# Kernel optimization log

Hardware: AMD Instinct MI355X
Metric: run time of the kernel (lower is better)

## Reference

```python
import jax, jax.numpy as jnp
import numpy as np
import math

B, S, OBS, ACT = 64, 256, 96, 29
D, H, L, FF = 512, 8, 8, 2048
HD = D // H
EPS = 1e-5

def _ln(x, g, b):
    m = jnp.mean(x, axis=-1, keepdims=True)
    v = jnp.mean((x - m) ** 2, axis=-1, keepdims=True)
    return (x - m) * jax.lax.rsqrt(v + EPS) * g + b

def _pos_encoding():
    pos = jnp.arange(S, dtype=jnp.float32)[:, None]
    div = jnp.exp(jnp.arange(0, D, 2, dtype=jnp.float32) * (-math.log(10000.0) / D))
    pe = jnp.zeros((S, D), dtype=jnp.float32)
    pe = pe.at[:, 0::2].set(jnp.sin(pos * div))
    pe = pe.at[:, 1::2].set(jnp.cos(pos * div))
    return pe

def setup_inputs() -> dict:
    key = jax.random.key(0)
    ks = iter(jax.random.split(key, 64))
    def w(shape, scale=0.02):
        return jax.random.normal(next(ks), shape, dtype=jnp.float32) * scale
    inp = {
        "observations": jax.random.normal(next(ks), (B, S, OBS), dtype=jnp.float32),
        "W_in": w((OBS, D)), "b_in": jnp.zeros((D,)),
        "g_in": jnp.ones((D,)), "be_in": jnp.zeros((D,)),
        "Wq": w((L, D, D)), "bq": jnp.zeros((L, D)),
        "Wk": w((L, D, D)), "bk": jnp.zeros((L, D)),
        "Wv": w((L, D, D)), "bv": jnp.zeros((L, D)),
        "Wo": w((L, D, D)), "bo": jnp.zeros((L, D)),
        "g1": jnp.ones((L, D)), "be1": jnp.zeros((L, D)),
        "W1": w((L, D, FF)), "b1": jnp.zeros((L, FF)),
        "W2": w((L, FF, D)), "b2": jnp.zeros((L, D)),
        "g2": jnp.ones((L, D)), "be2": jnp.zeros((L, D)),
        "Wp1": w((D, D // 2)), "bp1": jnp.zeros((D // 2,)),
        "gp1": jnp.ones((D // 2,)), "bep1": jnp.zeros((D // 2,)),
        "Wp2": w((D // 2, D // 4)), "bp2": jnp.zeros((D // 4,)),
        "gp2": jnp.ones((D // 4,)), "bep2": jnp.zeros((D // 4,)),
        "Wp3": w((D // 4, ACT)), "bp3": jnp.zeros((ACT,)),
        "action_scale": jnp.ones((ACT,)), "action_bias": jnp.zeros((ACT,)),
    }
    return inp

def _forward(observations, W_in, b_in, g_in, be_in, Wq, bq, Wk, bk, Wv, bv, Wo, bo,
             g1, be1, W1, b1, W2, b2, g2, be2,
             Wp1, bp1, gp1, bep1, Wp2, bp2, gp2, bep2, Wp3, bp3,
             action_scale, action_bias):
    gelu = lambda x: jax.nn.gelu(x, approximate=False)
    # input projection + LN + GELU (dropout = identity in eval)
    x = gelu(_ln(observations @ W_in + b_in, g_in, be_in))
    x = x + _pos_encoding()[None, :, :]  # [B,S,D]
    scale = 1.0 / math.sqrt(HD)
    for l in range(L):
        q = (x @ Wq[l] + bq[l]).reshape(B, S, H, HD)
        k = (x @ Wk[l] + bk[l]).reshape(B, S, H, HD)
        v = (x @ Wv[l] + bv[l]).reshape(B, S, H, HD)
        scores = jnp.einsum('bqhd,bkhd->bhqk', q, k) * scale
        attn = jax.nn.softmax(scores, axis=-1)
        o = jnp.einsum('bhqk,bkhd->bqhd', attn, v).reshape(B, S, D)
        x = _ln(x + (o @ Wo[l] + bo[l]), g1[l], be1[l])
        h = gelu(x @ W1[l] + b1[l])
        x = _ln(x + (h @ W2[l] + b2[l]), g2[l], be2[l])
    y = gelu(_ln(x @ Wp1 + bp1, gp1, bep1))
    y = gelu(_ln(y @ Wp2 + bp2, gp2, bep2))
    actions = jnp.tanh(y @ Wp3 + bp3)
    return actions * action_scale + action_bias

def reference(observations, W_in, b_in, g_in, be_in, Wq, bq, Wk, bk, Wv, bv, Wo, bo,
              g1, be1, W1, b1, W2, b2, g2, be2,
              Wp1, bp1, gp1, bep1, Wp2, bp2, gp2, bep2, Wp3, bp3,
              action_scale, action_bias):
    return _forward(observations, W_in, b_in, g_in, be_in, Wq, bq, Wk, bk, Wv, bv, Wo, bo,
                    g1, be1, W1, b1, W2, b2, g2, be2,
                    Wp1, bp1, gp1, bep1, Wp2, bp2, gp2, bep2, Wp3, bp3,
                    action_scale, action_bias)
```

## Files before the change

### kernel.cpp

```cpp
#include <hip/hip_runtime.h>

typedef unsigned short u16;
typedef unsigned int u32;
typedef __attribute__((ext_vector_type(8))) __bf16 bf16x8;
typedef __attribute__((ext_vector_type(4))) float f32x4;

#define B_ 64
#define S_ 256
#define OBS_ 96
#define ACT_ 29
#define D_ 512
#define H_ 8
#define L_ 8
#define FF_ 2048
#define HD_ 64
#define NTOK (B_ * S_)
#define QKV3 (3 * D_)

__device__ __forceinline__ u16 f2bf(float f) {
    u32 u = __float_as_uint(f);
    u += 0x7FFFu + ((u >> 16) & 1u);
    return (u16)(u >> 16);
}
__device__ __forceinline__ float bf2f(u16 h) {
    return __uint_as_float(((u32)h) << 16);
}
__device__ __forceinline__ u16 f2h(float f) {
    _Float16 h = (_Float16)f;
    u16 u; __builtin_memcpy(&u, &h, 2); return u;
}
__device__ __forceinline__ float h2f(u16 u) {
    _Float16 h; __builtin_memcpy(&h, &u, 2); return (float)h;
}
__device__ __forceinline__ float gelu_f(float x) {
    const float k1 = 2.3022121f;
    const float k2 = 0.10294451f;
    float x2 = x * x;
    float arg = x * __builtin_fmaf(x2, k2, k1);
    float e = exp2f(arg);
    float r = __builtin_amdgcn_rcpf(1.0f + e);
    return __builtin_fmaf(-x, r, x);
}
__device__ __forceinline__ void gld_lds16(const u16* g, u16* l) {
    __builtin_amdgcn_global_load_lds(
        (const __attribute__((address_space(1))) unsigned int*)g,
        (__attribute__((address_space(3))) unsigned int*)l, 16, 0, 0);
}

__global__ __launch_bounds__(256) void transpose_bf16_kernel(
    const float* __restrict__ src, u16* __restrict__ dst, int K, int N,
    size_t srcStride, size_t dstStride)
{
    __shared__ float tile[32][33];
    int n0 = blockIdx.x * 32, k0 = blockIdx.y * 32;
    const float* s = src + (size_t)blockIdx.z * srcStride;
    u16* d = dst + (size_t)blockIdx.z * dstStride;
    int tx = threadIdx.x, ty = threadIdx.y;
    for (int i = 0; i < 32; i += 8)
        tile[ty + i][tx] = s[(size_t)(k0 + ty + i) * N + n0 + tx];
    __syncthreads();
    for (int i = 0; i < 32; i += 8)
        d[(size_t)(n0 + ty + i) * K + k0 + tx] = f2bf(tile[tx][ty + i]);
}

__global__ __launch_bounds__(256) void concat_bias_kernel(
    const float* __restrict__ bq, const float* __restrict__ bk,
    const float* __restrict__ bv, float* __restrict__ dst)
{
    int i = blockIdx.x * 256 + threadIdx.x;
    int l = i / QKV3, r = i - l * QKV3;
    float v;
    if (r < D_)            v = bq[l * D_ + r];
    else if (r < 2 * D_)   v = bk[l * D_ + r - D_];
    else                   v = bv[l * D_ + r - 2 * D_];
    dst[i] = v;
}

__global__ __launch_bounds__(256) void in_gemm_kernel(
    const float* __restrict__ obs, const float* __restrict__ Win,
    const float* __restrict__ b_in, float* __restrict__ outp)
{
    __shared__ float As[OBS_][68];
    __shared__ float Bs[OBS_][68];
    int m0 = blockIdx.y * 64, n0 = blockIdx.x * 64;
    int t = threadIdx.x;
    #pragma unroll
    for (int i = 0; i < 24; i++) {
        int idx = i * 256 + t;
        int m = idx / OBS_, kk = idx - m * OBS_;
        As[kk][m] = obs[(size_t)(m0 + m) * OBS_ + kk];
    }
    #pragma unroll
    for (int i = 0; i < 24; i++) {
        int idx = i * 256 + t;
        int kk = idx >> 6, n = idx & 63;
        Bs[kk][n] = Win[(size_t)kk * D_ + n0 + n];
    }
    __syncthreads();
    int tm = t >> 4, tn = t & 15;
    float acc[4][4] = {};
    for (int kk = 0; kk < OBS_; kk++) {
        float4 a = *(const float4*)&As[kk][tm * 4];
        float4 b = *(const float4*)&Bs[kk][tn * 4];
        const float av[4] = {a.x, a.y, a.z, a.w};
        const float bv[4] = {b.x, b.y, b.z, b.w};
        #pragma unroll
        for (int r = 0; r < 4; r++)
            #pragma unroll
            for (int c = 0; c < 4; c++) acc[r][c] += av[r] * bv[c];
    }
    #pragma unroll
    for (int r = 0; r < 4; r++)
        #pragma unroll
        for (int c = 0; c < 4; c++) {
            int col = n0 + tn * 4 + c;
            outp[(size_t)(m0 + tm * 4 + r) * D_ + col] = acc[r][c] + b_in[col];
        }
}

template <int EPI, int TN, bool SPLITK>
__global__ __launch_bounds__(256, 3) void gemm_bt_kernel(
    const u16* __restrict__ A, const u16* __restrict__ BT,
    const float* __restrict__ bias, void* __restrict__ C,
    void* __restrict__ C2, int M, int N, int K, int kLen)
{
    constexpr int NI = TN / 32;
    constexpr int NB = TN / 32;
    __shared__ __align__(16) u16 smem[128 * 64 + TN * 64];
    u16* As = smem;
    u16* Bs = smem + 128 * 64;
    int bx = blockIdx.x;
    int m0 = (bx & 127) * 128, n0 = (bx >> 7) * TN;
    int z = SPLITK ? blockIdx.z : 0;
    int kStart = z * kLen;
    int t = threadIdx.x;
    int lane = t & 63, w = t >> 6;
    int wm = w >> 1, wn = w & 1;
    int l15 = lane & 15, quad = lane >> 4;

    int offC[4]; u16* lA[4];
    #pragma unroll
    for (int i = 0; i < 4; i++) {
        int ci = t + i * 256;
        int r = ci >> 3, s = ci & 7, gc = s ^ (r & 7);
        offC[i] = r * K + gc * 8;
        lA[i] = &As[ci * 8];
    }
    const u16* Abase = A + (size_t)m0 * K + kStart;
    const u16* Bbase = BT + (size_t)n0 * K + kStart;

    int aoff[2][4], boff[2][NI];
    #pragma unroll
    for (int kh = 0; kh < 2; kh++) {
        #pragma unroll
        for (int mi = 0; mi < 4; mi++) {
            int row = wm * 64 + mi * 16 + l15;
            aoff[kh][mi] = row * 64 + (((kh * 4 + quad) ^ (row & 7)) * 8);
        }
        #pragma unroll
        for (int ni = 0; ni < NI; ni++) {
            int row = wn * (TN / 2) + ni * 16 + l15;
            boff[kh][ni] = row * 64 + (((kh * 4 + quad) ^ (row & 7)) * 8);
        }
    }

    f32x4 acc[4][NI];
    f32x4 zero = {0.f, 0.f, 0.f, 0.f};
    #pragma unroll
    for (int mi = 0; mi < 4; mi++)
        #pragma unroll
        for (int ni = 0; ni < NI; ni++) acc[mi][ni] = zero;

    for (int kk = 0; kk < kLen; kk += 64) {
        __syncthreads();
        #pragma unroll
        for (int i = 0; i < 4; i++) gld_lds16(Abase + offC[i], lA[i]);
        #pragma unroll
        for (int i = 0; i < NB; i++) gld_lds16(Bbase + offC[i], lA[i] + 128 * 64);
        Abase += 64; Bbase += 64;
        __syncthreads();
        #pragma unroll
        for (int kh = 0; kh < 2; kh++) {
            bf16x8 a[4], b[NI];
            #pragma unroll
            for (int mi = 0; mi < 4; mi++)
                a[mi] = *(const bf16x8*)&As[aoff[kh][mi]];
            #pragma unroll
            for (int ni = 0; ni < NI; ni++)
                b[ni] = *(const bf16x8*)&Bs[boff[kh][ni]];
            #pragma unroll
            for (int mi = 0; mi < 4; mi++)
                #pragma unroll
                for (int ni = 0; ni < NI; ni++)
                    acc[mi][ni] = __builtin_amdgcn_mfma_f32_16x16x32_bf16(
                        a[mi], b[ni], acc[mi][ni], 0, 0, 0);
        }
    }

    bool partial = SPLITK && (z == 1);
    if (EPI == 2) {
        #pragma unroll
        for (int ni = 0; ni < NI; ni++) {
            int col = n0 + wn * (TN / 2) + ni * 16 + l15;
            float bv = partial ? 0.f : bias[col];
            #pragma unroll
            for (int mi = 0; mi < 4; mi++) {
                int rbase = m0 + wm * 64 + mi * 16 + quad * 4;
                f32x4 v = acc[mi][ni];
                #pragma unroll
                for (int r = 0; r < 4; r++)
                    ((float*)C)[(size_t)(rbase + r) * N + col] = v[r] + bv;
            }
        }
    } else {
        __syncthreads();
        u16* Ct = smem;
        #pragma unroll
        for (int ni = 0; ni < NI; ni++) {
            int colt = wn * (TN / 2) + ni * 16 + l15;
            float bv = partial ? 0.f : bias[n0 + colt];
            #pragma unroll
            for (int mi = 0; mi < 4; mi++) {
                int rbase = wm * 64 + mi * 16 + quad * 4;
                f32x4 v = acc[mi][ni];
                #pragma unroll
                for (int r = 0; r < 4; r++) {
                    float y = v[r] + bv;
                    if (EPI == 1) y = gelu_f(y);
                    u16 hv = (EPI == 3) ? f2h(y) : f2bf(y);
                    int row = rbase + r;
                    int cc = colt >> 3;
                    Ct[row * TN + (((cc ^ (row & 7)) * 8) | (colt & 7))] = hv;
                }
            }
        }
        __syncthreads();
        u16* dst = partial ? (u16*)C2 : (u16*)C;
        constexpr int CPR = TN / 8;
        #pragma unroll
        for (int i = 0; i < TN / 16; i++) {
            int ch = t + i * 256;
            int row = ch / CPR, cc = ch % CPR;
            uint4 vv = *(const uint4*)&Ct[row * TN + ((cc ^ (row & 7)) * 8)];
            *(uint4*)(dst + (size_t)(m0 + row) * N + n0 + cc * 8) = vv;
        }
    }
}

__global__ __launch_bounds__(256) void attn_kernel(
    const u16* __restrict__ qkv, u16* __restrict__ o)
{
    __shared__ __align__(16) u16 kvs[S_ * HD_];
    __shared__ __align__(16) u16 P[4 * 16 * S_];
    int bx = blockIdx.x;
    int qc = bx & 3;
    int h = (bx >> 2) & 7;
    int b = bx >> 5;
    int t = threadIdx.x;
    int lane = t & 63, w = t >> 6;
    int l15 = lane & 15, quad = lane >> 4;
    size_t rowb = (size_t)b * S_;

    {
        const u16* src = qkv + (rowb + t) * QKV3 + D_ + h * HD_;
        int sw = t & 7;
        #pragma unroll
        for (int j = 0; j < 8; j++)
            *(uint4*)&kvs[t * HD_ + ((j ^ sw) * 8)] = *(const uint4*)(src + j * 8);
    }
    bf16x8 aQ[2];
    {
        int qrow = qc * 64 + w * 16 + l15;
        const u16* src = qkv + (rowb + qrow) * QKV3 + h * HD_ + quad * 8;
        aQ[0] = *(const bf16x8*)(src);
        aQ[1] = *(const bf16x8*)(src + 32);
    }
    __syncthreads();

    f32x4 sc[16];
    #pragma unroll
    for (int nc = 0; nc < 16; nc++) {
        f32x4 acc = {0.f, 0.f, 0.f, 0.f};
        int row = nc * 16 + l15;
        int s0 = quad ^ (row & 7);
        bf16x8 b0 = *(const bf16x8*)&kvs[row * HD_ + s0 * 8];
        bf16x8 b1 = *(const bf16x8*)&kvs[row * HD_ + (s0 ^ 4) * 8];
        acc = __builtin_amdgcn_mfma_f32_16x16x32_bf16(aQ[0], b0, acc, 0, 0, 0);
        acc = __builtin_amdgcn_mfma_f32_16x16x32_bf16(aQ[1], b1, acc, 0, 0, 0);
        sc[nc] = acc;
    }
    const float scale = 0.125f;
    float rmax[4], rinv[4];
    #pragma unroll
    for (int r = 0; r < 4; r++) {
        float mx = -1e30f;
        #pragma unroll
        for (int nc = 0; nc < 16; nc++) mx = fmaxf(mx, sc[nc][r]);
        for (int off = 1; off < 16; off <<= 1) mx = fmaxf(mx, __shfl_xor(mx, off));
        rmax[r] = mx * scale;
    }
    #pragma unroll
    for (int r = 0; r < 4; r++) {
        float sum = 0.f;
        #pragma unroll
        for (int nc = 0; nc < 16; nc++) {
            float p = __expf(sc[nc][r] * scale - rmax[r]);
            sc[nc][r] = p;
            sum += p;
        }
        for (int off = 1; off < 16; off <<= 1) sum += __shfl_xor(sum, off);
        rinv[r] = 1.0f / sum;
    }
    #pragma unroll
    for (int nc = 0; nc < 16; nc++)
        #pragma unroll
        for (int r = 0; r < 4; r++) {
            int prow = quad * 4 + r;
            int col = nc * 16 + l15;
            int slot = (col >> 3) ^ (prow & 7);
            P[w * 4096 + prow * 256 + slot * 8 + (col & 7)] =
                f2bf(sc[nc][r] * rinv[r]);
        }
    __syncthreads();

    {
        const u16* src = qkv + (rowb + t) * QKV3 + 2 * D_ + h * HD_;
        int chunkc = t >> 3, bytec = t & 7;
        #pragma unroll
        for (int dj = 0; dj < 8; dj++) {
            uint4 x = *(const uint4*)(src + dj * 8);
            const u16* xs = (const u16*)&x;
            #pragma unroll
            for (int i = 0; i < 8; i++) {
                int vrow = dj * 8 + i;
                kvs[vrow * 256 + ((chunkc ^ (vrow & 7)) * 8) + bytec] = xs[i];
            }
        }
    }
    __syncthreads();

    f32x4 accO[4];
    f32x4 zero = {0.f, 0.f, 0.f, 0.f};
    #pragma unroll
    for (int nt = 0; nt < 4; nt++) accO[nt] = zero;
    for (int ks = 0; ks < 8; ks++) {
        int ch = ks * 4 + quad;
        bf16x8 aP = *(const bf16x8*)&P[w * 4096 + l15 * 256 + ((ch ^ (l15 & 7)) * 8)];
        #pragma unroll
        for (int nt = 0; nt < 4; nt++) {
            int vrow = nt * 16 + l15;
            bf16x8 bV = *(const bf16x8*)&kvs[vrow * 256 + ((ch ^ (vrow & 7)) * 8)];
            accO[nt] = __builtin_amdgcn_mfma_f32_16x16x32_bf16(aP, bV, accO[nt], 0, 0, 0);
        }
    }
    __syncthreads();
    u16* Ot = P;
    #pragma unroll
    for (int nt = 0; nt < 4; nt++)
        #pragma unroll
        for (int r = 0; r < 4; r++) {
            int row = w * 16 + quad * 4 + r;
            int col = nt * 16 + l15;
            int cc = col >> 3;
            Ot[row * 64 + (((cc ^ (row & 7)) * 8) | (col & 7))] = f2bf(accO[nt][r]);
        }
    __syncthreads();
    #pragma unroll
    for (int i = 0; i < 2; i++) {
        int ch = t + i * 256;
        int row = ch >> 3, cc = ch & 7;
        uint4 vv = *(const uint4*)&Ot[row * 64 + ((cc ^ (row & 7)) * 8)];
        *(uint4*)(o + (rowb + qc * 64 + row) * D_ + h * HD_ + cc * 8) = vv;
    }
}

template <int WIDTH, int INK, bool RES, bool GELU, bool PE, bool SUM2>
__global__ __launch_bounds__(WIDTH) void ln_kernel(
    const void* __restrict__ in, const void* __restrict__ in2,
    const u16* __restrict__ res,
    const float* __restrict__ g, const float* __restrict__ b,
    u16* __restrict__ out)
{
    __shared__ float rs[8], rq[8];
    int row = blockIdx.x;
    int t = threadIdx.x;
    size_t base = (size_t)row * WIDTH;
    float v = (INK == 0) ? ((const float*)in)[base + t]
                         : h2f(((const u16*)in)[base + t]);
    if (SUM2) v += (INK == 0) ? ((const float*)in2)[base + t]
                              : h2f(((const u16*)in2)[base + t]);
    if (RES) v += bf2f(res[base + t]);
    float sm = v, sq = v * v;
    for (int off = 32; off; off >>= 1) {
        sm += __shfl_xor(sm, off);
        sq += __shfl_xor(sq, off);
    }
    constexpr int NW = WIDTH / 64;
    if ((t & 63) == 0) { rs[t >> 6] = sm; rq[t >> 6] = sq; }
    __syncthreads();
    float ts = 0.f, tq = 0.f;
    #pragma unroll
    for (int i = 0; i < NW; i++) { ts += rs[i]; tq += rq[i]; }
    float mean = ts / (float)WIDTH;
    float var = tq / (float)WIDTH - mean * mean;
    float rstd = rsqrtf(var + 1e-5f);
    float y = (v - mean) * rstd * g[t] + b[t];
    if (GELU) y = gelu_f(y);
    if (PE) {
        const float c = -9.210340371976184f / (float)D_;
        int s = row & (S_ - 1);
        int i2 = t >> 1;
        float ang = (float)s * __expf((float)(2 * i2) * c);
        y += (t & 1) ? __cosf(ang) : __sinf(ang);
    }
    out[base + t] = f2bf(y);
}

__global__ __launch_bounds__(256) void head_kernel(
    const u16* __restrict__ y2, const float* __restrict__ W,
    const float* __restrict__ bias, const float* __restrict__ scl,
    const float* __restrict__ bs, float* __restrict__ out)
{
    __shared__ float Ws[128 * ACT_];
    __shared__ u16 Ys[8 * 128];
    int t = threadIdx.x;
    for (int i = t; i < 128 * ACT_; i += 256) Ws[i] = W[i];
    int r0 = blockIdx.x * 8;
    for (int i = t; i < 8 * 128; i += 256) Ys[i] = y2[(size_t)r0 * 128 + i];
    __syncthreads();
    int lr = t >> 5, c = t & 31;
    if (c < ACT_) {
        float acc = bias[c];
        for (int kk = 0; kk < 128; kk++)
            acc += bf2f(Ys[lr * 128 + kk]) * Ws[kk * ACT_ + c];
        float y = tanhf(acc);
        out[(size_t)(r0 + lr) * ACT_ + c] = y * scl[c] + bs[c];
    }
}

extern "C" void kernel_launch(void* const* d_in, const int* in_sizes, int n_in,
                              void* d_out, int out_size, void* d_ws, size_t ws_size,
                              hipStream_t stream)
{
    const float* obs   = (const float*)d_in[0];
    const float* W_in  = (const float*)d_in[1];
    const float* b_in  = (const float*)d_in[2];
    const float* g_in  = (const float*)d_in[3];
    const float* be_in = (const float*)d_in[4];
    const float* Wq  = (const float*)d_in[5];
    const float* bq  = (const float*)d_in[6];
    const float* Wk  = (const float*)d_in[7];
    const float* bk  = (const float*)d_in[8];
    const float* Wv  = (const float*)d_in[9];
    const float* bv  = (const float*)d_in[10];
    const float* Wo  = (const float*)d_in[11];
    const float* bo  = (const float*)d_in[12];
    const float* g1  = (const float*)d_in[13];
    const float* be1 = (const float*)d_in[14];
    const float* W1  = (const float*)d_in[15];
    const float* b1  = (const float*)d_in[16];
    const float* W2  = (const float*)d_in[17];
    const float* b2  = (const float*)d_in[18];
    const float* g2  = (const float*)d_in[19];
    const float* be2 = (const float*)d_in[20];
    const float* Wp1  = (const float*)d_in[21];
    const float* bp1  = (const float*)d_in[22];
    const float* gp1  = (const float*)d_in[23];
    const float* bep1 = (const float*)d_in[24];
    const float* Wp2  = (const float*)d_in[25];
    const float* bp2  = (const float*)d_in[26];
    const float* gp2  = (const float*)d_in[27];
    const float* bep2 = (const float*)d_in[28];
    const float* Wp3  = (const float*)d_in[29];
    const float* bp3  = (const float*)d_in[30];
    const float* ascl = (const float*)d_in[31];
    const float* abias = (const float*)d_in[32];

    char* ws = (char*)d_ws;
    size_t off = 0;
    auto alloc = [&](size_t bytes) {
        void* p = ws + off;
        off += (bytes + 255) & ~(size_t)255;
        return p;
    };
    u16* WQKVT = (u16*)alloc((size_t)L_ * QKV3 * D_ * 2);
    u16* WOT   = (u16*)alloc((size_t)L_ * D_ * D_ * 2);
    u16* W1T   = (u16*)alloc((size_t)L_ * D_ * FF_ * 2);
    u16* W2T   = (u16*)alloc((size_t)L_ * FF_ * D_ * 2);
    u16* WP1T  = (u16*)alloc((size_t)D_ * (D_ / 2) * 2);
    u16* WP2T  = (u16*)alloc((size_t)(D_ / 2) * (D_ / 4) * 2);
    float* bqkv = (float*)alloc((size_t)L_ * QKV3 * 4);
    u16* x_bf = (u16*)alloc((size_t)NTOK * D_ * 2);
    float* tmp = (float*)alloc((size_t)NTOK * D_ * 4);
    char* regionA = (char*)alloc((size_t)NTOK * FF_ * 2);
    size_t base_need = off;
    char* tmp2 = ws + base_need;
    bool split = (ws_size >= base_need + (size_t)NTOK * D_ * 2);
    (void)in_sizes; (void)n_in; (void)out_size;

    u16* qkvbuf = (u16*)(regionA);
    u16* obuf = (u16*)(regionA + (size_t)NTOK * QKV3 * 2);
    u16* hbuf = (u16*)(regionA);
    u16* y1_bf = (u16*)(regionA);
    u16* y2_bf = (u16*)(regionA + (32u << 20));

    dim3 tb(32, 8);
    size_t DD = (size_t)D_ * D_;
    transpose_bf16_kernel<<<dim3(16, 16, L_), tb, 0, stream>>>(
        Wq, WQKVT, D_, D_, DD, (size_t)QKV3 * D_);
    transpose_bf16_kernel<<<dim3(16, 16, L_), tb, 0, stream>>>(
        Wk, WQKVT + DD, D_, D_, DD, (size_t)QKV3 * D_);
    transpose_bf16_kernel<<<dim3(16, 16, L_), tb, 0, stream>>>(
        Wv, WQKVT + 2 * DD, D_, D_, DD, (size_t)QKV3 * D_);
    transpose_bf16_kernel<<<dim3(16, 16, L_), tb, 0, stream>>>(
        Wo, WOT, D_, D_, DD, DD);
    transpose_bf16_kernel<<<dim3(64, 16, L_), tb, 0, stream>>>(
        W1, W1T, D_, FF_, (size_t)D_ * FF_, (size_t)D_ * FF_);
    transpose_bf16_kernel<<<dim3(16, 64, L_), tb, 0, stream>>>(
        W2, W2T, FF_, D_, (size_t)D_ * FF_, (size_t)D_ * FF_);
    transpose_bf16_kernel<<<dim3(8, 16, 1), tb, 0, stream>>>(
        Wp1, WP1T, D_, D_ / 2, 0, 0);
    transpose_bf16_kernel<<<dim3(4, 8, 1), tb, 0, stream>>>(
        Wp2, WP2T, D_ / 2, D_ / 4, 0, 0);
    concat_bias_kernel<<<L_ * QKV3 / 256, 256, 0, stream>>>(bq, bk, bv, bqkv);

    in_gemm_kernel<<<dim3(D_ / 64, NTOK / 64), 256, 0, stream>>>(
        obs, W_in, b_in, tmp);
    ln_kernel<D_, 0, false, true, true, false><<<NTOK, D_, 0, stream>>>(
        tmp, nullptr, nullptr, g_in, be_in, x_bf);

    const int MG = NTOK / 128;
    for (int l = 0; l < L_; l++) {
        const u16* wqkvt = WQKVT + (size_t)l * QKV3 * D_;
        const u16* wot = WOT + (size_t)l * DD;
        const u16* w1t = W1T + (size_t)l * D_ * FF_;
        const u16* w2t = W2T + (size_t)l * FF_ * D_;

        gemm_bt_kernel<0, 128, false><<<MG * (QKV3 / 128), 256, 0, stream>>>(
            x_bf, wqkvt, bqkv + l * QKV3, qkvbuf, nullptr, NTOK, QKV3, D_, D_);
        attn_kernel<<<B_ * H_ * (S_ / 64), 256, 0, stream>>>(qkvbuf, obuf);
        if (split) {
            gemm_bt_kernel<3, 128, true><<<dim3(MG * 4, 1, 2), 256, 0, stream>>>(
                obuf, wot, bo + l * D_, tmp, tmp2, NTOK, D_, D_, D_ / 2);
            ln_kernel<D_, 1, true, false, false, true><<<NTOK, D_, 0, stream>>>(
                tmp, tmp2, x_bf, g1 + l * D_, be1 + l * D_, x_bf);
        } else {
            gemm_bt_kernel<2, 128, false><<<MG * 4, 256, 0, stream>>>(
                obuf, wot, bo + l * D_, tmp, nullptr, NTOK, D_, D_, D_);
            ln_kernel<D_, 0, true, false, false, false><<<NTOK, D_, 0, stream>>>(
                tmp, nullptr, x_bf, g1 + l * D_, be1 + l * D_, x_bf);
        }
        gemm_bt_kernel<1, 128, false><<<MG * (FF_ / 128), 256, 0, stream>>>(
            x_bf, w1t, b1 + l * FF_, hbuf, nullptr, NTOK, FF_, D_, D_);
        if (split) {
            gemm_bt_kernel<3, 128, true><<<dim3(MG * 4, 1, 2), 256, 0, stream>>>(
                hbuf, w2t, b2 + l * D_, tmp, tmp2, NTOK, D_, FF_, FF_ / 2);
            ln_kernel<D_, 1, true, false, false, true><<<NTOK, D_, 0, stream>>>(
                tmp, tmp2, x_bf, g2 + l * D_, be2 + l * D_, x_bf);
        } else {
            gemm_bt_kernel<2, 128, false><<<MG * 4, 256, 0, stream>>>(
                hbuf, w2t, b2 + l * D_, tmp, nullptr, NTOK, D_, FF_, FF_);
            ln_kernel<D_, 0, true, false, false, false><<<NTOK, D_, 0, stream>>>(
                tmp, nullptr, x_bf, g2 + l * D_, be2 + l * D_, x_bf);
        }
    }

    if (split) {
        gemm_bt_kernel<3, 64, true><<<dim3(MG * 4, 1, 2), 256, 0, stream>>>(
            x_bf, WP1T, bp1, tmp, tmp2, NTOK, D_ / 2, D_, D_ / 2);
        ln_kernel<D_ / 2, 1, false, true, false, true><<<NTOK, D_ / 2, 0, stream>>>(
            tmp, tmp2, nullptr, gp1, bep1, y1_bf);
        gemm_bt_kernel<3, 64, true><<<dim3(MG * 2, 1, 2), 256, 0, stream>>>(
            y1_bf, WP2T, bp2, tmp, tmp2, NTOK, D_ / 4, D_ / 2, D_ / 4);
        ln_kernel<D_ / 4, 1, false, true, false, true><<<NTOK, D_ / 4, 0, stream>>>(
            tmp, tmp2, nullptr, gp2, bep2, y2_bf);
    } else {
        gemm_bt_kernel<2, 64, false><<<MG * 4, 256, 0, stream>>>(
            x_bf, WP1T, bp1, tmp, nullptr, NTOK, D_ / 2, D_, D_);
        ln_kernel<D_ / 2, 0, false, true, false, false><<<NTOK, D_ / 2, 0, stream>>>(
            tmp, nullptr, nullptr, gp1, bep1, y1_bf);
        gemm_bt_kernel<2, 64, false><<<MG * 2, 256, 0, stream>>>(
            y1_bf, WP2T, bp2, tmp, nullptr, NTOK, D_ / 4, D_ / 2, D_ / 2);
        ln_kernel<D_ / 4, 0, false, true, false, false><<<NTOK, D_ / 4, 0, stream>>>(
            tmp, nullptr, nullptr, gp2, bep2, y2_bf);
    }
    head_kernel<<<NTOK / 8, 256, 0, stream>>>(
        y2_bf, Wp3, bp3, ascl, abias, (float*)d_out);
}
```

Baseline: 2.196 ms.

## Vectorize layernorm, defer softmax normalization, use native bf16 convert and paired GELU

LayerNorm now processes four elements per thread with vector loads and stores and packs several rows into each 256-thread block. This cuts block count and the shared-memory reduction for narrow rows. Attention applies the softmax reciprocal to the 64-wide output instead of to every probability. f2bf uses the hardware bf16 conversion, and the GEMM epilogue computes GELU on float pairs to encourage packed math. These are several unrelated micro-optimizations on non-GEMM costs, with small rounding differences (P is stored unnormalized in bf16).

```diff
diff --git a/kernel.cpp b/kernel.cpp
--- a/kernel.cpp
+++ b/kernel.cpp
@@ -4,6 +4,7 @@
 typedef unsigned int u32;
 typedef __attribute__((ext_vector_type(8))) __bf16 bf16x8;
 typedef __attribute__((ext_vector_type(4))) float f32x4;
+typedef __attribute__((ext_vector_type(2))) float f32x2;
 
 #define B_ 64
 #define S_ 256
@@ -18,9 +19,8 @@
 #define QKV3 (3 * D_)
 
 __device__ __forceinline__ u16 f2bf(float f) {
-    u32 u = __float_as_uint(f);
-    u += 0x7FFFu + ((u >> 16) & 1u);
-    return (u16)(u >> 16);
+    __bf16 h = (__bf16)f;
+    u16 u; __builtin_memcpy(&u, &h, 2); return u;
 }
 __device__ __forceinline__ float bf2f(u16 h) {
     return __uint_as_float(((u32)h) << 16);
@@ -40,6 +40,20 @@
     float e = exp2f(arg);
     float r = __builtin_amdgcn_rcpf(1.0f + e);
     return __builtin_fmaf(-x, r, x);
+}
+__device__ __forceinline__ f32x2 gelu2(f32x2 x) {
+    const float k1 = 2.3022121f;
+    const float k2 = 0.10294451f;
+    f32x2 x2 = x * x;
+    f32x2 arg = x * (x2 * k2 + k1);
+    f32x2 e;
+    e.x = exp2f(arg.x);
+    e.y = exp2f(arg.y);
+    f32x2 one_e = e + 1.0f;
+    f32x2 r;
+    r.x = __builtin_amdgcn_rcpf(one_e.x);
+    r.y = __builtin_amdgcn_rcpf(one_e.y);
+    return x - x * r;
 }
 __device__ __forceinline__ void gld_lds16(const u16* g, u16* l) {
     __builtin_amdgcn_global_load_lds(
@@ -223,11 +237,15 @@
             for (int mi = 0; mi < 4; mi++) {
                 int rbase = wm * 64 + mi * 16 + quad * 4;
                 f32x4 v = acc[mi][ni];
+                f32x2 y01 = {v[0], v[1]};
+                f32x2 y23 = {v[2], v[3]};
+                y01 = y01 + bv;
+                y23 = y23 + bv;
+                if (EPI == 1) { y01 = gelu2(y01); y23 = gelu2(y23); }
+                const float ys[4] = {y01.x, y01.y, y23.x, y23.y};
                 #pragma unroll
                 for (int r = 0; r < 4; r++) {
-                    float y = v[r] + bv;
-                    if (EPI == 1) y = gelu_f(y);
-                    u16 hv = (EPI == 3) ? f2h(y) : f2bf(y);
+                    u16 hv = (EPI == 3) ? f2h(ys[r]) : f2bf(ys[r]);
                     int row = rbase + r;
                     int cc = colt >> 3;
                     Ct[row * TN + (((cc ^ (row & 7)) * 8) | (colt & 7))] = hv;
@@ -318,8 +336,7 @@
             int prow = quad * 4 + r;
             int col = nc * 16 + l15;
             int slot = (col >> 3) ^ (prow & 7);
-            P[w * 4096 + prow * 256 + slot * 8 + (col & 7)] =
-                f2bf(sc[nc][r] * rinv[r]);
+            P[w * 4096 + prow * 256 + slot * 8 + (col & 7)] = f2bf(sc[nc][r]);
         }
     __syncthreads();
 
@@ -362,7 +379,8 @@
             int row = w * 16 + quad * 4 + r;
             int col = nt * 16 + l15;
             int cc = col >> 3;
-            Ot[row * 64 + (((cc ^ (row & 7)) * 8) | (col & 7))] = f2bf(accO[nt][r]);
+            Ot[row * 64 + (((cc ^ (row & 7)) * 8) | (col & 7))] =
+                f2bf(accO[nt][r] * rinv[r]);
         }
     __syncthreads();
     #pragma unroll
@@ -375,45 +393,93 @@
 }
 
 template <int WIDTH, int INK, bool RES, bool GELU, bool PE, bool SUM2>
-__global__ __launch_bounds__(WIDTH) void ln_kernel(
+__global__ __launch_bounds__(256) void ln_kernel(
     const void* __restrict__ in, const void* __restrict__ in2,
     const u16* __restrict__ res,
     const float* __restrict__ g, const float* __restrict__ b,
     u16* __restrict__ out)
 {
-    __shared__ float rs[8], rq[8];
-    int row = blockIdx.x;
+    constexpr int T = WIDTH / 4;
+    constexpr int R = 256 / T;
+    __shared__ float rs[R][2], rq[R][2];
     int t = threadIdx.x;
-    size_t base = (size_t)row * WIDTH;
-    float v = (INK == 0) ? ((const float*)in)[base + t]
-                         : h2f(((const u16*)in)[base + t]);
-    if (SUM2) v += (INK == 0) ? ((const float*)in2)[base + t]
-                              : h2f(((const u16*)in2)[base + t]);
-    if (RES) v += bf2f(res[base + t]);
-    float sm = v, sq = v * v;
-    for (int off = 32; off; off >>= 1) {
-        sm += __shfl_xor(sm, off);
-        sq += __shfl_xor(sq, off);
-    }
-    constexpr int NW = WIDTH / 64;
-    if ((t & 63) == 0) { rs[t >> 6] = sm; rq[t >> 6] = sq; }
-    __syncthreads();
-    float ts = 0.f, tq = 0.f;
-    #pragma unroll
-    for (int i = 0; i < NW; i++) { ts += rs[i]; tq += rq[i]; }
-    float mean = ts / (float)WIDTH;
-    float var = tq / (float)WIDTH - mean * mean;
+    int r = t / T, j = t % T;
+    int row = blockIdx.x * R + r;
+    size_t base = (size_t)row * WIDTH + j * 4;
+    float v[4];
+    if (INK == 0) {
+        float4 x = *(const float4*)((const float*)in + base);
+        v[0] = x.x; v[1] = x.y; v[2] = x.z; v[3] = x.w;
+    } else {
+        uint2 x = *(const uint2*)((const u16*)in + base);
+        const u16* xs = (const u16*)&x;
+        #pragma unroll
+        for (int i = 0; i < 4; i++) v[i] = h2f(xs[i]);
+    }
+    if (SUM2) {
+        if (INK == 0) {
+            float4 x = *(const float4*)((const float*)in2 + base);
+            v[0] += x.x; v[1] += x.y; v[2] += x.z; v[3] += x.w;
+        } else {
+            uint2 x = *(const uint2*)((const u16*)in2 + base);
+            const u16* xs = (const u16*)&x;
+            #pragma unroll
+            for (int i = 0; i < 4; i++) v[i] += h2f(xs[i]);
+        }
+    }
+    if (RES) {
+        uint2 x = *(const uint2*)(res + base);
+        const u16* xs = (const u16*)&x;
+        #pragma unroll
+        for (int i = 0; i < 4; i++) v[i] += bf2f(xs[i]);
+    }
+    float sm = v[0] + v[1] + v[2] + v[3];
+    float sq = v[0] * v[0] + v[1] * v[1] + v[2] * v[2] + v[3] * v[3];
+    if constexpr (T >= 64) {
+        #pragma unroll
+        for (int off = 32; off; off >>= 1) {
+            sm += __shfl_xor(sm, off);
+            sq += __shfl_xor(sq, off);
+        }
+    } else {
+        #pragma unroll
+        for (int off = 16; off; off >>= 1) {
+            sm += __shfl_xor(sm, off, 32);
+            sq += __shfl_xor(sq, off, 32);
+        }
+    }
+    if constexpr (T == 128) {
+        if ((t & 63) == 0) { rs[r][(t >> 6) & 1] = sm; rq[r][(t >> 6) & 1] = sq; }
+        __syncthreads();
+        sm = rs[r][0] + rs[r][1];
+        sq = rq[r][0] + rq[r][1];
+    }
+    float mean = sm / (float)WIDTH;
+    float var = sq / (float)WIDTH - mean * mean;
     float rstd = rsqrtf(var + 1e-5f);
-    float y = (v - mean) * rstd * g[t] + b[t];
-    if (GELU) y = gelu_f(y);
-    if (PE) {
-        const float c = -9.210340371976184f / (float)D_;
-        int s = row & (S_ - 1);
-        int i2 = t >> 1;
-        float ang = (float)s * __expf((float)(2 * i2) * c);
-        y += (t & 1) ? __cosf(ang) : __sinf(ang);
-    }
-    out[base + t] = f2bf(y);
+    float4 gv = *(const float4*)(g + j * 4);
+    float4 bv = *(const float4*)(b + j * 4);
+    const float gs[4] = {gv.x, gv.y, gv.z, gv.w};
+    const float bs[4] = {bv.x, bv.y, bv.z, bv.w};
+    u16 o4[4];
+    #pragma unroll
+    for (int i = 0; i < 4; i++) {
+        float y = (v[i] - mean) * rstd * gs[i] + bs[i];
+        if (GELU) y = gelu_f(y);
+        if (PE) {
+            const float c = -9.210340371976184f / (float)D_;
+            int s = row & (S_ - 1);
+            int col = j * 4 + i;
+            int i2 = col >> 1;
+            float ang = (float)s * __expf((float)(2 * i2) * c);
+            y += (col & 1) ? __cosf(ang) : __sinf(ang);
+        }
+        o4[i] = f2bf(y);
+    }
+    uint2 ov;
+    ov.x = (u32)o4[0] | ((u32)o4[1] << 16);
+    ov.y = (u32)o4[2] | ((u32)o4[3] << 16);
+    *(uint2*)(out + base) = ov;
 }
 
 __global__ __launch_bounds__(256) void head_kernel(
@@ -526,7 +592,7 @@
 
     in_gemm_kernel<<<dim3(D_ / 64, NTOK / 64), 256, 0, stream>>>(
         obs, W_in, b_in, tmp);
-    ln_kernel<D_, 0, false, true, true, false><<<NTOK, D_, 0, stream>>>(
+    ln_kernel<D_, 0, false, true, true, false><<<NTOK / 2, 256, 0, stream>>>(
         tmp, nullptr, nullptr, g_in, be_in, x_bf);
 
     const int MG = NTOK / 128;
@@ -542,12 +608,12 @@
         if (split) {
             gemm_bt_kernel<3, 128, true><<<dim3(MG * 4, 1, 2), 256, 0, stream>>>(
                 obuf, wot, bo + l * D_, tmp, tmp2, NTOK, D_, D_, D_ / 2);
-            ln_kernel<D_, 1, true, false, false, true><<<NTOK, D_, 0, stream>>>(
+            ln_kernel<D_, 1, true, false, false, true><<<NTOK / 2, 256, 0, stream>>>(
                 tmp, tmp2, x_bf, g1 + l * D_, be1 + l * D_, x_bf);
         } else {
             gemm_bt_kernel<2, 128, false><<<MG * 4, 256, 0, stream>>>(
                 obuf, wot, bo + l * D_, tmp, nullptr, NTOK, D_, D_, D_);
-            ln_kernel<D_, 0, true, false, false, false><<<NTOK, D_, 0, stream>>>(
+            ln_kernel<D_, 0, true, false, false, false><<<NTOK / 2, 256, 0, stream>>>(
                 tmp, nullptr, x_bf, g1 + l * D_, be1 + l * D_, x_bf);
         }
         gemm_bt_kernel<1, 128, false><<<MG * (FF_ / 128), 256, 0, stream>>>(
@@ -555,12 +621,12 @@
         if (split) {
             gemm_bt_kernel<3, 128, true><<<dim3(MG * 4, 1, 2), 256, 0, stream>>>(
                 hbuf, w2t, b2 + l * D_, tmp, tmp2, NTOK, D_, FF_, FF_ / 2);
-            ln_kernel<D_, 1, true, false, false, true><<<NTOK, D_, 0, stream>>>(
+            ln_kernel<D_, 1, true, false, false, true><<<NTOK / 2, 256, 0, stream>>>(
                 tmp, tmp2, x_bf, g2 + l * D_, be2 + l * D_, x_bf);
         } else {
             gemm_bt_kernel<2, 128, false><<<MG * 4, 256, 0, stream>>>(
                 hbuf, w2t, b2 + l * D_, tmp, nullptr, NTOK, D_, FF_, FF_);
-            ln_kernel<D_, 0, true, false, false, false><<<NTOK, D_, 0, stream>>>(
+            ln_kernel<D_, 0, true, false, false, false><<<NTOK / 2, 256, 0, stream>>>(
                 tmp, nullptr, x_bf, g2 + l * D_, be2 + l * D_, x_bf);
         }
     }
@@ -568,20 +634,20 @@
     if (split) {
         gemm_bt_kernel<3, 64, true><<<dim3(MG * 4, 1, 2), 256, 0, stream>>>(
             x_bf, WP1T, bp1, tmp, tmp2, NTOK, D_ / 2, D_, D_ / 2);
-        ln_kernel<D_ / 2, 1, false, true, false, true><<<NTOK, D_ / 2, 0, stream>>>(
+        ln_kernel<D_ / 2, 1, false, true, false, true><<<NTOK / 4, 256, 0, stream>>>(
             tmp, tmp2, nullptr, gp1, bep1, y1_bf);
         gemm_bt_kernel<3, 64, true><<<dim3(MG * 2, 1, 2), 256, 0, stream>>>(
             y1_bf, WP2T, bp2, tmp, tmp2, NTOK, D_ / 4, D_ / 2, D_ / 4);
-        ln_kernel<D_ / 4, 1, false, true, false, true><<<NTOK, D_ / 4, 0, stream>>>(
+        ln_kernel<D_ / 4, 1, false, true, false, true><<<NTOK / 8, 256, 0, stream>>>(
             tmp, tmp2, nullptr, gp2, bep2, y2_bf);
     } else {
         gemm_bt_kernel<2, 64, false><<<MG * 4, 256, 0, stream>>>(
             x_bf, WP1T, bp1, tmp, nullptr, NTOK, D_ / 2, D_, D_);
-        ln_kernel<D_ / 2, 0, false, true, false, false><<<NTOK, D_ / 2, 0, stream>>>(
+        ln_kernel<D_ / 2, 0, false, true, false, false><<<NTOK / 4, 256, 0, stream>>>(
             tmp, nullptr, nullptr, gp1, bep1, y1_bf);
         gemm_bt_kernel<2, 64, false><<<MG * 2, 256, 0, stream>>>(
             y1_bf, WP2T, bp2, tmp, nullptr, NTOK, D_ / 4, D_ / 2, D_ / 2);
-        ln_kernel<D_ / 4, 0, false, true, false, false><<<NTOK, D_ / 4, 0, stream>>>(
+        ln_kernel<D_ / 4, 0, false, true, false, false><<<NTOK / 8, 256, 0, stream>>>(
             tmp, nullptr, nullptr, gp2, bep2, y2_bf);
     }
     head_kernel<<<NTOK / 8, 256, 0, stream>>>(
```

Measured after the change: 1.967 ms. 10.4% less time.
